# Optimization experiments

Measured on AMD Instinct MI355X. Metric: run time of the kernel, lower is better.

## Reference

```python
import jax, jax.numpy as jnp
import numpy as np

EMBED_DIM = 512
NUM_HEADS = 8
HEAD_DIM = EMBED_DIM // NUM_HEADS
GRID_SHAPE = (48, 48)
WINDOW = (16, 16)
BATCH = 2
SEQ = GRID_SHAPE[0] * GRID_SHAPE[1]
NEG = float(np.finfo(np.float16).min)  # matches torch.finfo(torch.float16).min fill


def build_window_mask():
    # replicates: indices = np.indices(grid).flatten(1).T; dist = |i-j|*2; all(dist < window)
    idx = np.indices(GRID_SHAPE).reshape(len(GRID_SHAPE), -1).T  # [N, 2]
    dist = np.abs(idx[:, None, :] - idx[None, :, :]) * 2          # [N, N, 2]
    mask = np.all(dist < np.array(WINDOW)[None, None, :], axis=-1)  # [N, N] bool
    return jnp.asarray(mask)


def setup_inputs() -> dict:
    key = jax.random.key(0)
    ks = jax.random.split(key, 11)
    s = 1.0 / np.sqrt(EMBED_DIM)
    inp = {
        "x_q": jax.random.normal(ks[0], (BATCH, SEQ, EMBED_DIM), jnp.float32),
        "x_k": jax.random.normal(ks[1], (BATCH, SEQ, EMBED_DIM), jnp.float32),
        "x_v": jax.random.normal(ks[2], (BATCH, SEQ, EMBED_DIM), jnp.float32),
        "Wq": jax.random.normal(ks[3], (EMBED_DIM, EMBED_DIM), jnp.float32) * s,
        "bq": jnp.zeros((EMBED_DIM,), jnp.float32),
        "Wk": jax.random.normal(ks[4], (EMBED_DIM, EMBED_DIM), jnp.float32) * s,
        "bk": jnp.zeros((EMBED_DIM,), jnp.float32),
        "Wv": jax.random.normal(ks[5], (EMBED_DIM, EMBED_DIM), jnp.float32) * s,
        "bv": jnp.zeros((EMBED_DIM,), jnp.float32),
        "Wo": jax.random.normal(ks[6], (EMBED_DIM, EMBED_DIM), jnp.float32) * s,
        "bo": jnp.zeros((EMBED_DIM,), jnp.float32),
        "attn_mask": build_window_mask(),
    }
    return inp


def reference(x_q, x_k, x_v, Wq, bq, Wk, bk, Wv, bv, Wo, bo, attn_mask):
    B, S, E = x_q.shape
    H, D = NUM_HEADS, HEAD_DIM

    def proj(x, W, b):
        y = x @ W.T + b                         # [B,S,E]
        return y.reshape(B, S, H, D).transpose(0, 2, 1, 3)  # [B,H,S,D]

    q = proj(x_q, Wq, bq)
    k = proj(x_k, Wk, bk)
    v = proj(x_v, Wv, bv)

    scores = jnp.einsum("bhqd,bhkd->bhqk", q, k) / np.sqrt(D)
    # Windowed branch: per-row gather over allowed keys + softmax == dense
    # softmax with disallowed keys masked to a huge negative value.
    scores = jnp.where(attn_mask[None, None, :, :], scores, NEG)
    probs = jax.nn.softmax(scores, axis=-1)     # dropout=0.0 -> identity
    context = jnp.einsum("bhqk,bhkd->bhqd", probs, v)
    context = context.transpose(0, 2, 1, 3).reshape(B, S, E)
    out = context @ Wo.T + bo
    return out
```

## Files before the change

### kernel.cpp

```cpp
#include <hip/hip_runtime.h>

typedef __attribute__((ext_vector_type(8))) short short8;
typedef __attribute__((ext_vector_type(4))) float f32x4;
typedef __attribute__((ext_vector_type(2))) unsigned int u32x2;
typedef __attribute__((ext_vector_type(4))) unsigned int u32x4;

#define DEV __device__ __forceinline__

#define QH_E 0L
#define KH_E 2359296L
#define VT_E 4718592L
#define CTX_E 7077888L

#define LOG2E 1.4426950408889634f

#define BARRIER() __builtin_amdgcn_s_barrier()
#define SCHED0() __builtin_amdgcn_sched_barrier(0)

DEV unsigned short f2bf(float f) {
  unsigned int x = __float_as_uint(f);
  x = (x + 0x7fffu + ((x >> 16) & 1u)) >> 16;
  return (unsigned short)x;
}

DEV unsigned int pk2(float a, float b) {
  unsigned int r;
  asm("v_cvt_pk_bf16_f32 %0, %1, %2" : "=v"(r) : "v"(a), "v"(b));
  return r;
}

DEV void gl2lds16(const unsigned short* g, unsigned short* l) {
  __builtin_amdgcn_global_load_lds(
      (const __attribute__((address_space(1))) unsigned int*)g,
      (__attribute__((address_space(3))) unsigned int*)l, 16, 0, 0);
}

DEV f32x4 mfma16(short8 a, short8 b, f32x4 c) {
  return __builtin_amdgcn_mfma_f32_16x16x32_bf16(a, b, c, 0, 0, 0);
}

DEV void gemm_qkv(const float* __restrict__ A, const float* __restrict__ W,
                  int m0, int n0, unsigned short* ldsA, unsigned short* ldsB,
                  f32x4 acc[2][4]) {
  const int tid = threadIdx.x;
  const int lane = tid & 63, wvv = tid >> 6;
  const int g = lane >> 4, qi = lane & 15;
  const int wr = wvv >> 1, wc = wvv & 1;
  const int c8 = tid & 7, rbase = tid >> 3;
  const int j8 = (c8 ^ (rbase & 7)) * 8;
  f32x4 ra[2][2][2];
  f32x4 rw[4][2];
#pragma unroll
  for (int mi = 0; mi < 2; ++mi)
#pragma unroll
    for (int ni = 0; ni < 4; ++ni) {
      f32x4 z = {0.f, 0.f, 0.f, 0.f};
      acc[mi][ni] = z;
    }
#define QLA(kt) do {                                                          \
    const int k0_ = (kt) * 64;                                                \
    _Pragma("unroll")                                                         \
    for (int it = 0; it < 2; ++it) {                                          \
      const float* p = A + (long)(m0 + it * 32 + rbase) * 512 + k0_ + j8;     \
      ra[(kt) & 1][it][0] = *(const f32x4*)p;                                 \
      ra[(kt) & 1][it][1] = *(const f32x4*)(p + 4);                           \
    }                                                                         \
  } while (0)
#define QLB(kt) do {                                                          \
    const int k0_ = (kt) * 64;                                                \
    _Pragma("unroll")                                                         \
    for (int it = 0; it < 4; ++it) {                                          \
      const float* p = W + (long)(n0 + it * 32 + rbase) * 512 + k0_ + j8;     \
      rw[it][0] = *(const f32x4*)p;                                           \
      rw[it][1] = *(const f32x4*)(p + 4);                                     \
    }                                                                         \
  } while (0)
#define QWA(bi, set) do {                                                     \
    _Pragma("unroll")                                                         \
    for (int it = 0; it < 2; ++it) {                                          \
      u32x4 v_;                                                               \
      v_.x = pk2(ra[set][it][0].x, ra[set][it][0].y);                         \
      v_.y = pk2(ra[set][it][0].z, ra[set][it][0].w);                         \
      v_.z = pk2(ra[set][it][1].x, ra[set][it][1].y);                         \
      v_.w = pk2(ra[set][it][1].z, ra[set][it][1].w);                         \
      *(u32x4*)(ldsA + (bi) * 4096 + (it * 256 + tid) * 8) = v_;              \
    }                                                                         \
  } while (0)
#define QWB(bi) do {                                                          \
    _Pragma("unroll")                                                         \
    for (int it = 0; it < 4; ++it) {                                          \
      u32x4 v_;                                                               \
      v_.x = pk2(rw[it][0].x, rw[it][0].y);                                   \
      v_.y = pk2(rw[it][0].z, rw[it][0].w);                                   \
      v_.z = pk2(rw[it][1].x, rw[it][1].y);                                   \
      v_.w = pk2(rw[it][1].z, rw[it][1].w);                                   \
      *(u32x4*)(ldsB + (bi) * 8192 + (it * 256 + tid) * 8) = v_;              \
    }                                                                         \
  } while (0)
  QLA(0); QLB(0);
  QWA(0, 0); QWB(0);
  QLA(1); QLB(1);
  asm volatile("s_waitcnt lgkmcnt(0)" ::: "memory");
  BARRIER();
  SCHED0();
#pragma unroll
  for (int kt = 0; kt < 8; ++kt) {
    const unsigned short* La = ldsA + (kt & 1) * 4096;
    const unsigned short* Lb = ldsB + (kt & 1) * 8192;
    __builtin_amdgcn_s_setprio(1);
#pragma unroll
    for (int kk = 0; kk < 2; ++kk) {
      short8 af[2], bfr[4];
#pragma unroll
      for (int mi = 0; mi < 2; ++mi) {
        int row = 32 * wr + 16 * mi + qi;
        int c16 = (4 * kk + g) ^ (qi & 7);
        af[mi] = *(const short8*)(La + row * 64 + c16 * 8);
      }
#pragma unroll
      for (int ni = 0; ni < 4; ++ni) {
        int row = 64 * wc + 16 * ni + qi;
        int c16 = (4 * kk + g) ^ (qi & 7);
        bfr[ni] = *(const short8*)(Lb + row * 64 + c16 * 8);
      }
#pragma unroll
      for (int mi = 0; mi < 2; ++mi)
#pragma unroll
        for (int ni = 0; ni < 4; ++ni)
          acc[mi][ni] = mfma16(af[mi], bfr[ni], acc[mi][ni]);
    }
    __builtin_amdgcn_s_setprio(0);
    SCHED0();
    if (kt < 7) { QWA((kt + 1) & 1, (kt + 1) & 1); QWB((kt + 1) & 1); }
    if (kt < 6) QLA(kt + 2);
    if (kt < 7) QLB(kt + 2);
    if (kt < 7) {
      asm volatile("s_waitcnt lgkmcnt(0)" ::: "memory");
      BARRIER();
      SCHED0();
    }
  }
#undef QLA
#undef QLB
#undef QWA
#undef QWB
}

DEV void gemm_o(const unsigned short* __restrict__ A, const float* __restrict__ W,
                int m0, int n0, unsigned short* ldsA, unsigned short* ldsB,
                f32x4 acc[2][2]) {
  const int tid = threadIdx.x;
  const int lane = tid & 63, wvv = tid >> 6;
  const int g = lane >> 4, qi = lane & 15;
  const int wr = wvv >> 1, wc = wvv & 1;
  const int c8 = tid & 7, rbase = tid >> 3;
  const int j8 = (c8 ^ (rbase & 7)) * 8;
  u32x4 rab[2][2];
  f32x4 rw[2][2][2];
#pragma unroll
  for (int mi = 0; mi < 2; ++mi)
#pragma unroll
    for (int ni = 0; ni < 2; ++ni) {
      f32x4 z = {0.f, 0.f, 0.f, 0.f};
      acc[mi][ni] = z;
    }
#define OLA(kt) do {                                                          \
    const int k0_ = (kt) * 64;                                                \
    _Pragma("unroll")                                                         \
    for (int it = 0; it < 2; ++it)                                            \
      rab[(kt) & 1][it] =                                                     \
          *(const u32x4*)(A + (long)(m0 + it * 32 + rbase) * 512 + k0_ + j8); \
  } while (0)
#define OLB(kt) do {                                                          \
    const int k0_ = (kt) * 64;                                                \
    _Pragma("unroll")                                                         \
    for (int it = 0; it < 2; ++it) {                                          \
      const float* p = W + (long)(n0 + it * 32 + rbase) * 512 + k0_ + j8;     \
      rw[(kt) & 1][it][0] = *(const f32x4*)p;                                 \
      rw[(kt) & 1][it][1] = *(const f32x4*)(p + 4);                           \
    }                                                                         \
  } while (0)
#define OW(kt) do {                                                           \
    const int b3_ = (kt) % 3, s_ = (kt) & 1;                                  \
    _Pragma("unroll")                                                         \
    for (int it = 0; it < 2; ++it)                                            \
      *(u32x4*)(ldsA + b3_ * 4096 + (it * 256 + tid) * 8) = rab[s_][it];      \
    _Pragma("unroll")                                                         \
    for (int it = 0; it < 2; ++it) {                                          \
      u32x4 v_;                                                               \
      v_.x = pk2(rw[s_][it][0].x, rw[s_][it][0].y);                           \
      v_.y = pk2(rw[s_][it][0].z, rw[s_][it][0].w);                           \
      v_.z = pk2(rw[s_][it][1].x, rw[s_][it][1].y);                           \
      v_.w = pk2(rw[s_][it][1].z, rw[s_][it][1].w);                           \
      *(u32x4*)(ldsB + b3_ * 4096 + (it * 256 + tid) * 8) = v_;               \
    }                                                                         \
  } while (0)
  OLA(0); OLB(0);
  OLA(1); OLB(1);
  OW(0);
  OLA(2); OLB(2);
  OW(1);
  OLA(3); OLB(3);
  asm volatile("s_waitcnt lgkmcnt(0)" ::: "memory");
  BARRIER();
  SCHED0();
#pragma unroll
  for (int kt = 0; kt < 8; ++kt) {
    const unsigned short* La = ldsA + (kt % 3) * 4096;
    const unsigned short* Lb = ldsB + (kt % 3) * 4096;
    __builtin_amdgcn_s_setprio(1);
#pragma unroll
    for (int kk = 0; kk < 2; ++kk) {
      short8 af[2], bfr[2];
#pragma unroll
      for (int mi = 0; mi < 2; ++mi) {
        int row = 32 * wr + 16 * mi + qi;
        int c16 = (4 * kk + g) ^ (qi & 7);
        af[mi] = *(const short8*)(La + row * 64 + c16 * 8);
      }
#pragma unroll
      for (int ni = 0; ni < 2; ++ni) {
        int row = 32 * wc + 16 * ni + qi;
        int c16 = (4 * kk + g) ^ (qi & 7);
        bfr[ni] = *(const short8*)(Lb + row * 64 + c16 * 8);
      }
#pragma unroll
      for (int mi = 0; mi < 2; ++mi)
#pragma unroll
        for (int ni = 0; ni < 2; ++ni)
          acc[mi][ni] = mfma16(af[mi], bfr[ni], acc[mi][ni]);
    }
    __builtin_amdgcn_s_setprio(0);
    SCHED0();
    if (kt < 6) OW(kt + 2);
    if (kt < 4) { OLA(kt + 4); OLB(kt + 4); }
    if (kt < 7) {
      asm volatile("s_waitcnt lgkmcnt(0)" ::: "memory");
      BARRIER();
      SCHED0();
    }
  }
#undef OLA
#undef OLB
#undef OW
}

__global__ __launch_bounds__(256, 3) void proj_qkv_kernel(
    const float* __restrict__ xq, const float* __restrict__ xk,
    const float* __restrict__ xv, const float* __restrict__ wqp,
    const float* __restrict__ wkp, const float* __restrict__ wvp,
    const float* __restrict__ bq, const float* __restrict__ bk,
    const float* __restrict__ bv, unsigned short* __restrict__ ws) {
  __shared__ unsigned short ldsA[2 * 4096];
  __shared__ unsigned short ldsB[2 * 8192];
  int f = blockIdx.x;
  int wid = (f & 7) * 108 + (f >> 3);
  const int z = wid / 288;
  const int rem = wid % 288;
  const int m0 = (rem >> 2) * 64, n0 = (rem & 3) * 128;
  const float *A, *W, *bias;
  unsigned short* dst;
  float oscale;
  int mode;
  if (z == 0)      { A = xq; W = wqp; bias = bq; oscale = 0.125f * LOG2E; dst = ws + QH_E; mode = 0; }
  else if (z == 1) { A = xk; W = wkp; bias = bk; oscale = 1.0f;           dst = ws + KH_E; mode = 0; }
  else             { A = xv; W = wvp; bias = bv; oscale = 1.0f;           dst = ws + VT_E; mode = 1; }
  f32x4 acc[2][4];
  gemm_qkv(A, W, m0, n0, ldsA, ldsB, acc);
  const int lane = threadIdx.x & 63, wvv = threadIdx.x >> 6;
  const int g = lane >> 4, qi = lane & 15;
  const int wr = wvv >> 1, wc = wvv & 1;
#pragma unroll
  for (int ni = 0; ni < 4; ++ni) {
    int n = n0 + 64 * wc + 16 * ni + qi;
    float bb = bias[n];
    int h = n >> 6, d = n & 63;
#pragma unroll
    for (int mi = 0; mi < 2; ++mi) {
      int m = m0 + 32 * wr + 16 * mi + 4 * g;
      int b = (m >= 2304) ? 1 : 0;
      int s = m - b * 2304;
      if (mode == 0) {
#pragma unroll
        for (int r = 0; r < 4; ++r) {
          float v = (acc[mi][ni][r] + bb) * oscale;
          dst[((long)((b * 8 + h) * 2304 + s + r)) * 64 + d] = f2bf(v);
        }
      } else {
        u32x2 o;
        o.x = pk2(acc[mi][ni][0] + bb, acc[mi][ni][1] + bb);
        o.y = pk2(acc[mi][ni][2] + bb, acc[mi][ni][3] + bb);
        *(u32x2*)(dst + ((long)((b * 8 + h) * 64 + d)) * 2304 + s) = o;
      }
    }
  }
}

__global__ __launch_bounds__(256, 3) void proj_out_kernel(
    const unsigned short* __restrict__ ws, const float* __restrict__ wop,
    const float* __restrict__ bo, float* __restrict__ out) {
  __shared__ unsigned short ldsA[3 * 4096];
  __shared__ unsigned short ldsB[3 * 4096];
  int f = blockIdx.x;
  int wid = (f & 7) * 72 + (f >> 3);
  const int m0 = (wid >> 3) * 64, n0 = (wid & 7) * 64;
  f32x4 acc[2][2];
  gemm_o(ws + CTX_E, wop, m0, n0, ldsA, ldsB, acc);
  const int lane = threadIdx.x & 63, wvv = threadIdx.x >> 6;
  const int g = lane >> 4, qi = lane & 15;
  const int wr = wvv >> 1, wc = wvv & 1;
#pragma unroll
  for (int ni = 0; ni < 2; ++ni) {
    int n = n0 + 32 * wc + 16 * ni + qi;
    float bb = bo[n];
#pragma unroll
    for (int mi = 0; mi < 2; ++mi) {
#pragma unroll
      for (int r = 0; r < 4; ++r) {
        int m = m0 + 32 * wr + 16 * mi + 4 * g + r;
        out[(long)m * 512 + n] = acc[mi][ni][r] + bb;
      }
    }
  }
}

__global__ __launch_bounds__(192) void attn_kernel(unsigned short* __restrict__ ws) {
  __shared__ unsigned short ldsKV[3 * 7168];
  __shared__ unsigned short ldsP[3][16][72];
  __shared__ unsigned short ldsDum[512];
  const int tid = threadIdx.x;
  const int lane = tid & 63, wv = tid >> 6;
  const int g = lane >> 4, qi = lane & 15;
  int f = blockIdx.x;
  int wid = (f & 7) * 96 + (f >> 3);
  const int bh = wid / 48, r = wid - 48 * bh;
  const int ci = wv * 16 + qi;
  const unsigned short* Kh = ws + KH_E + (long)bh * 2304 * 64;
  const unsigned short* Vt = ws + VT_E + (long)bh * 64 * 2304;
  const int q = r * 48 + ci;
  const unsigned short* qp = ws + QH_E + ((long)bh * 2304 + q) * 64;
  f32x4 qraw0 = *(const f32x4*)(qp + 8 * g);
  f32x4 qraw1 = *(const f32x4*)(qp + 32 + 8 * g);
  asm volatile("" : "+v"(qraw0), "+v"(qraw1));
  short8 qf0 = __builtin_bit_cast(short8, qraw0);
  short8 qf1 = __builtin_bit_cast(short8, qraw1);
  float msk[12];
#pragma unroll
  for (int mb = 0; mb < 3; ++mb)
#pragma unroll
    for (int rr = 0; rr < 4; ++rr) {
      int cj = 16 * mb + 4 * g + rr;
      msk[mb * 4 + rr] = ((unsigned)(ci - cj + 7) <= 14u) ? 0.f : -1e30f;
    }
  {
    u32x2 z2; z2.x = 0u; z2.y = 0u;
    *(u32x2*)(&ldsP[wv][qi][48 + 4 * g]) = z2;
  }
  f32x4 cacc[4];
#pragma unroll
  for (int mb = 0; mb < 4; ++mb) { f32x4 z = {0.f, 0.f, 0.f, 0.f}; cacc[mb] = z; }
  float lrun = 0.f;

#define ASTAGE(bi, rj) do {                                                   \
    unsigned short* Lb_ = ldsKV + (bi) * 7168;                                \
    const unsigned short* Ks_ = Kh + (long)(rj) * 3072;                       \
    _Pragma("unroll")                                                         \
    for (int it = 0; it < 5; ++it) {                                          \
      int u = it * 192 + tid;                                                 \
      if (u < 384) {                                                          \
        int kr = u >> 3, c = u & 7, cs = c ^ (kr & 7);                        \
        gl2lds16(Ks_ + kr * 64 + cs * 8, Lb_ + u * 8);                        \
      } else if (u < 896) {                                                   \
        int v2 = u - 384;                                                     \
        int d = v2 >> 3, c = v2 & 7, cs = c ^ (d & 7);                        \
        long jb = (long)(rj) * 48 + cs * 8;                                   \
        if (jb > 2296) jb = 2296;                                             \
        gl2lds16(Vt + (long)d * 2304 + jb, Lb_ + u * 8);                      \
      } else {                                                                \
        gl2lds16(Kh + (u - 896) * 8, ldsDum + (u - 896) * 8);                 \
      }                                                                       \
    }                                                                         \
  } while (0)

#define AQK(KB, S) do {                                                       \
    const unsigned short* Kt_ = (KB);                                         \
    _Pragma("unroll")                                                         \
    for (int mb = 0; mb < 3; ++mb) { f32x4 z = {0.f,0.f,0.f,0.f}; S[mb] = z; }\
    __builtin_amdgcn_s_setprio(1);                                            \
    _Pragma("unroll")                                                         \
    for (int kk = 0; kk < 2; ++kk) {                                          \
      short8 qf_ = kk ? qf1 : qf0;                                            \
      _Pragma("unroll")                                                       \
      for (int mb = 0; mb < 3; ++mb) {                                        \
        int row = 16 * mb + qi;                                               \
        int c16 = (4 * kk + g) ^ (qi & 7);                                    \
        short8 ka = *(const short8*)(Kt_ + row * 64 + c16 * 8);               \
        S[mb] = mfma16(ka, qf_, S[mb]);                                       \
      }                                                                       \
    }                                                                         \
    __builtin_amdgcn_s_setprio(0);                                            \
  } while (0)

#define ASMPV(VB, S) do {                                                     \
    const unsigned short* Vm_ = (VB);                                         \
    unsigned int pw[6];                                                       \
    _Pragma("unroll")                                                         \
    for (int mb = 0; mb < 3; ++mb) {                                          \
      float p0 = __builtin_amdgcn_exp2f(S[mb][0] + msk[mb * 4 + 0]);          \
      float p1 = __builtin_amdgcn_exp2f(S[mb][1] + msk[mb * 4 + 1]);          \
      float p2 = __builtin_amdgcn_exp2f(S[mb][2] + msk[mb * 4 + 2]);          \
      float p3 = __builtin_amdgcn_exp2f(S[mb][3] + msk[mb * 4 + 3]);          \
      lrun += (p0 + p1) + (p2 + p3);                                          \
      pw[2 * mb] = pk2(p0, p1);                                               \
      pw[2 * mb + 1] = pk2(p2, p3);                                           \
    }                                                                         \
    _Pragma("unroll")                                                         \
    for (int mb = 0; mb < 3; ++mb) {                                          \
      u32x2 pv2; pv2.x = pw[2 * mb]; pv2.y = pw[2 * mb + 1];                  \
      *(u32x2*)(&ldsP[wv][qi][16 * mb + 4 * g]) = pv2;                        \
    }                                                                         \
    __builtin_amdgcn_s_setprio(1);                                            \
    _Pragma("unroll")                                                         \
    for (int kk = 0; kk < 2; ++kk) {                                          \
      short8 pb = *(const short8*)(&ldsP[wv][qi][32 * kk + 8 * g]);           \
      _Pragma("unroll")                                                       \
      for (int mb = 0; mb < 4; ++mb) {                                        \
        int row = 16 * mb + qi;                                               \
        int c16 = (4 * kk + g) ^ (qi & 7);                                    \
        short8 va = *(const short8*)(Vm_ + row * 64 + c16 * 8);               \
        cacc[mb] = mfma16(va, pb, cacc[mb]);                                  \
      }                                                                       \
    }                                                                         \
    __builtin_amdgcn_s_setprio(0);                                            \
  } while (0)

  const int rlo = (r > 7) ? r - 7 : 0;
  const int rhi = (r < 40) ? r + 7 : 47;
  const int nch = rhi - rlo + 1;
  f32x4 sE[3], sO[3];
  ASTAGE(0, rlo);
  ASTAGE(1, rlo + 1);
  asm volatile("s_waitcnt vmcnt(5)" ::: "memory");
  BARRIER();
  SCHED0();
  AQK(ldsKV, sE);
  int bc = 0;
  for (int t = 0; t < nch; t += 2) {
    const int b1 = (bc + 1 == 3) ? 0 : bc + 1;
    const int b2 = (b1 + 1 == 3) ? 0 : b1 + 1;
    asm volatile("s_waitcnt vmcnt(0)" ::: "memory");
    BARRIER();
    SCHED0();
    if (t + 2 < nch) ASTAGE(b2, rlo + t + 2);
    if (t + 1 < nch) AQK(ldsKV + b1 * 7168, sO);
    ASMPV(ldsKV + bc * 7168 + 3072, sE);
    if (t + 1 < nch) {
      asm volatile("s_waitcnt vmcnt(0)" ::: "memory");
      BARRIER();
      SCHED0();
      if (t + 3 < nch) ASTAGE(bc, rlo + t + 3);
      if (t + 2 < nch) AQK(ldsKV + b2 * 7168, sE);
      ASMPV(ldsKV + b1 * 7168 + 3072, sO);
    }
    bc = b2;
  }
#undef ASTAGE
#undef AQK
#undef ASMPV
  lrun += __shfl_xor(lrun, 16);
  lrun += __shfl_xor(lrun, 32);
  const float inv = 1.0f / lrun;
  unsigned short* ctx = ws + CTX_E;
  const int b2w = bh >> 3, h2 = bh & 7;
#pragma unroll
  for (int mb = 0; mb < 4; ++mb) {
    u32x2 o;
    o.x = pk2(cacc[mb][0] * inv, cacc[mb][1] * inv);
    o.y = pk2(cacc[mb][2] * inv, cacc[mb][3] * inv);
    long off = ((long)(b2w * 2304 + q)) * 512 + h2 * 64 + 16 * mb + 4 * g;
    *(u32x2*)(ctx + off) = o;
  }
}

extern "C" void kernel_launch(void* const* d_in, const int* in_sizes, int n_in,
                              void* d_out, int out_size, void* d_ws, size_t ws_size,
                              hipStream_t stream) {
  const float* xq = (const float*)d_in[0];
  const float* xk = (const float*)d_in[1];
  const float* xv = (const float*)d_in[2];
  const float* wq = (const float*)d_in[3];
  const float* bq = (const float*)d_in[4];
  const float* wk = (const float*)d_in[5];
  const float* bk = (const float*)d_in[6];
  const float* wv = (const float*)d_in[7];
  const float* bv = (const float*)d_in[8];
  const float* wo = (const float*)d_in[9];
  const float* bo = (const float*)d_in[10];
  unsigned short* ws = (unsigned short*)d_ws;
  float* out = (float*)d_out;

  proj_qkv_kernel<<<dim3(864), dim3(256), 0, stream>>>(xq, xk, xv, wq, wk, wv,
                                                       bq, bk, bv, ws);
  attn_kernel<<<dim3(768), dim3(192), 0, stream>>>(ws);
  proj_out_kernel<<<dim3(576), dim3(256), 0, stream>>>(ws, wo, bo, out);
}
```

Baseline: 58.76 us.

## Rewrite QKV projection as LDS-free single-wave kernel loading MFMA fragments directly

The QKV projection GEMM no longer stages tiles through double-buffered shared memory with barriers. Each 64-thread block now computes a 32x64 tile, loading fp32 operands from global memory straight into MFMA fragment layout, converting to bf16 in registers, and software-pipelining the loads over two register sets. This removes LDS traffic and block-wide synchronisation. In exchange, data reuse across waves is lost, so operands are re-read from global or L2 more often, and the per-lane loads are less coalesced.

Measured after the change: 122.6 us. +108.7%, slower.

```diff
diff --git a/kernel.cpp b/kernel.cpp
--- a/kernel.cpp
+++ b/kernel.cpp
@@ -39,111 +39,111 @@
   return __builtin_amdgcn_mfma_f32_16x16x32_bf16(a, b, c, 0, 0, 0);
 }
 
-DEV void gemm_qkv(const float* __restrict__ A, const float* __restrict__ W,
-                  int m0, int n0, unsigned short* ldsA, unsigned short* ldsB,
-                  f32x4 acc[2][4]) {
-  const int tid = threadIdx.x;
-  const int lane = tid & 63, wvv = tid >> 6;
+__global__ __launch_bounds__(64) void proj_qkv_kernel(
+    const float* __restrict__ xq, const float* __restrict__ xk,
+    const float* __restrict__ xv, const float* __restrict__ wqp,
+    const float* __restrict__ wkp, const float* __restrict__ wvp,
+    const float* __restrict__ bq, const float* __restrict__ bk,
+    const float* __restrict__ bv, unsigned short* __restrict__ ws) {
+  int f = blockIdx.x;
+  int wid = (f & 7) * 432 + (f >> 3);
+  const int z = wid / 1152;
+  const int rem = wid % 1152;
+  const int m0 = (rem >> 3) * 32, n0 = (rem & 7) * 64;
+  const float *A, *W, *bias;
+  unsigned short* dst;
+  float oscale;
+  int mode;
+  if (z == 0)      { A = xq; W = wqp; bias = bq; oscale = 0.125f * LOG2E; dst = ws + QH_E; mode = 0; }
+  else if (z == 1) { A = xk; W = wkp; bias = bk; oscale = 1.0f;           dst = ws + KH_E; mode = 0; }
+  else             { A = xv; W = wvp; bias = bv; oscale = 1.0f;           dst = ws + VT_E; mode = 1; }
+  const int lane = threadIdx.x;
   const int g = lane >> 4, qi = lane & 15;
-  const int wr = wvv >> 1, wc = wvv & 1;
-  const int c8 = tid & 7, rbase = tid >> 3;
-  const int j8 = (c8 ^ (rbase & 7)) * 8;
-  f32x4 ra[2][2][2];
-  f32x4 rw[4][2];
+  const float* Ab = A + (long)(m0 + qi) * 512 + 8 * g;
+  const float* Wb = W + (long)(n0 + qi) * 512 + 8 * g;
+  f32x4 acc[2][4];
 #pragma unroll
   for (int mi = 0; mi < 2; ++mi)
 #pragma unroll
     for (int ni = 0; ni < 4; ++ni) {
-      f32x4 z = {0.f, 0.f, 0.f, 0.f};
-      acc[mi][ni] = z;
-    }
-#define QLA(kt) do {                                                          \
-    const int k0_ = (kt) * 64;                                                \
-    _Pragma("unroll")                                                         \
-    for (int it = 0; it < 2; ++it) {                                          \
-      const float* p = A + (long)(m0 + it * 32 + rbase) * 512 + k0_ + j8;     \
-      ra[(kt) & 1][it][0] = *(const f32x4*)p;                                 \
-      ra[(kt) & 1][it][1] = *(const f32x4*)(p + 4);                           \
-    }                                                                         \
-  } while (0)
-#define QLB(kt) do {                                                          \
-    const int k0_ = (kt) * 64;                                                \
-    _Pragma("unroll")                                                         \
-    for (int it = 0; it < 4; ++it) {                                          \
-      const float* p = W + (long)(n0 + it * 32 + rbase) * 512 + k0_ + j8;     \
-      rw[it][0] = *(const f32x4*)p;                                           \
-      rw[it][1] = *(const f32x4*)(p + 4);                                     \
-    }                                                                         \
-  } while (0)
-#define QWA(bi, set) do {                                                     \
-    _Pragma("unroll")                                                         \
-    for (int it = 0; it < 2; ++it) {                                          \
+      f32x4 z4 = {0.f, 0.f, 0.f, 0.f};
+      acc[mi][ni] = z4;
+    }
+  f32x4 ea[2][2], ew[4][2], oa[2][2], ow[4][2];
+#define QLD(AR, WR, s) do {                                                   \
+    _Pragma("unroll")                                                         \
+    for (int mi = 0; mi < 2; ++mi) {                                          \
+      const float* p_ = Ab + mi * (16 * 512) + (s) * 32;                      \
+      AR[mi][0] = *(const f32x4*)p_;                                          \
+      AR[mi][1] = *(const f32x4*)(p_ + 4);                                    \
+    }                                                                         \
+    _Pragma("unroll")                                                         \
+    for (int ni = 0; ni < 4; ++ni) {                                          \
+      const float* p_ = Wb + ni * (16 * 512) + (s) * 32;                      \
+      WR[ni][0] = *(const f32x4*)p_;                                          \
+      WR[ni][1] = *(const f32x4*)(p_ + 4);                                    \
+    }                                                                         \
+  } while (0)
+#define QCM(AR, WR) do {                                                      \
+    short8 af_[2], bw_[4];                                                    \
+    _Pragma("unroll")                                                         \
+    for (int mi = 0; mi < 2; ++mi) {                                          \
       u32x4 v_;                                                               \
-      v_.x = pk2(ra[set][it][0].x, ra[set][it][0].y);                         \
-      v_.y = pk2(ra[set][it][0].z, ra[set][it][0].w);                         \
-      v_.z = pk2(ra[set][it][1].x, ra[set][it][1].y);                         \
-      v_.w = pk2(ra[set][it][1].z, ra[set][it][1].w);                         \
-      *(u32x4*)(ldsA + (bi) * 4096 + (it * 256 + tid) * 8) = v_;              \
-    }                                                                         \
-  } while (0)
-#define QWB(bi) do {                                                          \
-    _Pragma("unroll")                                                         \
-    for (int it = 0; it < 4; ++it) {                                          \
+      v_.x = pk2(AR[mi][0].x, AR[mi][0].y);                                   \
+      v_.y = pk2(AR[mi][0].z, AR[mi][0].w);                                   \
+      v_.z = pk2(AR[mi][1].x, AR[mi][1].y);                                   \
+      v_.w = pk2(AR[mi][1].z, AR[mi][1].w);                                   \
+      af_[mi] = __builtin_bit_cast(short8, v_);                               \
+    }                                                                         \
+    _Pragma("unroll")                                                         \
+    for (int ni = 0; ni < 4; ++ni) {                                          \
       u32x4 v_;                                                               \
-      v_.x = pk2(rw[it][0].x, rw[it][0].y);                                   \
-      v_.y = pk2(rw[it][0].z, rw[it][0].w);                                   \
-      v_.z = pk2(rw[it][1].x, rw[it][1].y);                                   \
-      v_.w = pk2(rw[it][1].z, rw[it][1].w);                                   \
-      *(u32x4*)(ldsB + (bi) * 8192 + (it * 256 + tid) * 8) = v_;              \
-    }                                                                         \
-  } while (0)
-  QLA(0); QLB(0);
-  QWA(0, 0); QWB(0);
-  QLA(1); QLB(1);
-  asm volatile("s_waitcnt lgkmcnt(0)" ::: "memory");
-  BARRIER();
-  SCHED0();
-#pragma unroll
-  for (int kt = 0; kt < 8; ++kt) {
-    const unsigned short* La = ldsA + (kt & 1) * 4096;
-    const unsigned short* Lb = ldsB + (kt & 1) * 8192;
-    __builtin_amdgcn_s_setprio(1);
-#pragma unroll
-    for (int kk = 0; kk < 2; ++kk) {
-      short8 af[2], bfr[4];
-#pragma unroll
-      for (int mi = 0; mi < 2; ++mi) {
-        int row = 32 * wr + 16 * mi + qi;
-        int c16 = (4 * kk + g) ^ (qi & 7);
-        af[mi] = *(const short8*)(La + row * 64 + c16 * 8);
+      v_.x = pk2(WR[ni][0].x, WR[ni][0].y);                                   \
+      v_.y = pk2(WR[ni][0].z, WR[ni][0].w);                                   \
+      v_.z = pk2(WR[ni][1].x, WR[ni][1].y);                                   \
+      v_.w = pk2(WR[ni][1].z, WR[ni][1].w);                                   \
+      bw_[ni] = __builtin_bit_cast(short8, v_);                               \
+    }                                                                         \
+    _Pragma("unroll")                                                         \
+    for (int mi = 0; mi < 2; ++mi)                                            \
+      _Pragma("unroll")                                                       \
+      for (int ni = 0; ni < 4; ++ni)                                          \
+        acc[mi][ni] = mfma16(af_[mi], bw_[ni], acc[mi][ni]);                  \
+  } while (0)
+  QLD(ea, ew, 0);
+#pragma unroll
+  for (int s = 0; s < 16; s += 2) {
+    QLD(oa, ow, s + 1);
+    QCM(ea, ew);
+    if (s + 2 < 16) QLD(ea, ew, s + 2);
+    QCM(oa, ow);
+  }
+#undef QLD
+#undef QCM
+#pragma unroll
+  for (int ni = 0; ni < 4; ++ni) {
+    int n = n0 + 16 * ni + qi;
+    float bb = bias[n];
+    int h = n >> 6, d = n & 63;
+#pragma unroll
+    for (int mi = 0; mi < 2; ++mi) {
+      int m = m0 + 16 * mi + 4 * g;
+      int b = (m >= 2304) ? 1 : 0;
+      int s = m - b * 2304;
+      if (mode == 0) {
+#pragma unroll
+        for (int r = 0; r < 4; ++r) {
+          float v = (acc[mi][ni][r] + bb) * oscale;
+          dst[((long)((b * 8 + h) * 2304 + s + r)) * 64 + d] = f2bf(v);
+        }
+      } else {
+        u32x2 o;
+        o.x = pk2(acc[mi][ni][0] + bb, acc[mi][ni][1] + bb);
+        o.y = pk2(acc[mi][ni][2] + bb, acc[mi][ni][3] + bb);
+        *(u32x2*)(dst + ((long)((b * 8 + h) * 64 + d)) * 2304 + s) = o;
       }
-#pragma unroll
-      for (int ni = 0; ni < 4; ++ni) {
-        int row = 64 * wc + 16 * ni + qi;
-        int c16 = (4 * kk + g) ^ (qi & 7);
-        bfr[ni] = *(const short8*)(Lb + row * 64 + c16 * 8);
-      }
-#pragma unroll
-      for (int mi = 0; mi < 2; ++mi)
-#pragma unroll
-        for (int ni = 0; ni < 4; ++ni)
-          acc[mi][ni] = mfma16(af[mi], bfr[ni], acc[mi][ni]);
-    }
-    __builtin_amdgcn_s_setprio(0);
-    SCHED0();
-    if (kt < 7) { QWA((kt + 1) & 1, (kt + 1) & 1); QWB((kt + 1) & 1); }
-    if (kt < 6) QLA(kt + 2);
-    if (kt < 7) QLB(kt + 2);
-    if (kt < 7) {
-      asm volatile("s_waitcnt lgkmcnt(0)" ::: "memory");
-      BARRIER();
-      SCHED0();
-    }
-  }
-#undef QLA
-#undef QLB
-#undef QWA
-#undef QWB
+    }
+  }
 }
 
 DEV void gemm_o(const unsigned short* __restrict__ A, const float* __restrict__ W,
@@ -243,57 +243,6 @@
 #undef OLA
 #undef OLB
 #undef OW
-}
-
-__global__ __launch_bounds__(256, 3) void proj_qkv_kernel(
-    const float* __restrict__ xq, const float* __restrict__ xk,
-    const float* __restrict__ xv, const float* __restrict__ wqp,
-    const float* __restrict__ wkp, const float* __restrict__ wvp,
-    const float* __restrict__ bq, const float* __restrict__ bk,
-    const float* __restrict__ bv, unsigned short* __restrict__ ws) {
-  __shared__ unsigned short ldsA[2 * 4096];
-  __shared__ unsigned short ldsB[2 * 8192];
-  int f = blockIdx.x;
-  int wid = (f & 7) * 108 + (f >> 3);
-  const int z = wid / 288;
-  const int rem = wid % 288;
-  const int m0 = (rem >> 2) * 64, n0 = (rem & 3) * 128;
-  const float *A, *W, *bias;
-  unsigned short* dst;
-  float oscale;
-  int mode;
-  if (z == 0)      { A = xq; W = wqp; bias = bq; oscale = 0.125f * LOG2E; dst = ws + QH_E; mode = 0; }
-  else if (z == 1) { A = xk; W = wkp; bias = bk; oscale = 1.0f;           dst = ws + KH_E; mode = 0; }
-  else             { A = xv; W = wvp; bias = bv; oscale = 1.0f;           dst = ws + VT_E; mode = 1; }
-  f32x4 acc[2][4];
-  gemm_qkv(A, W, m0, n0, ldsA, ldsB, acc);
-  const int lane = threadIdx.x & 63, wvv = threadIdx.x >> 6;
-  const int g = lane >> 4, qi = lane & 15;
-  const int wr = wvv >> 1, wc = wvv & 1;
-#pragma unroll
-  for (int ni = 0; ni < 4; ++ni) {
-    int n = n0 + 64 * wc + 16 * ni + qi;
-    float bb = bias[n];
-    int h = n >> 6, d = n & 63;
-#pragma unroll
-    for (int mi = 0; mi < 2; ++mi) {
-      int m = m0 + 32 * wr + 16 * mi + 4 * g;
-      int b = (m >= 2304) ? 1 : 0;
-      int s = m - b * 2304;
-      if (mode == 0) {
-#pragma unroll
-        for (int r = 0; r < 4; ++r) {
-          float v = (acc[mi][ni][r] + bb) * oscale;
-          dst[((long)((b * 8 + h) * 2304 + s + r)) * 64 + d] = f2bf(v);
-        }
-      } else {
-        u32x2 o;
-        o.x = pk2(acc[mi][ni][0] + bb, acc[mi][ni][1] + bb);
-        o.y = pk2(acc[mi][ni][2] + bb, acc[mi][ni][3] + bb);
-        *(u32x2*)(dst + ((long)((b * 8 + h) * 64 + d)) * 2304 + s) = o;
-      }
-    }
-  }
 }
 
 __global__ __launch_bounds__(256, 3) void proj_out_kernel(
@@ -499,7 +448,7 @@
   unsigned short* ws = (unsigned short*)d_ws;
   float* out = (float*)d_out;
 
-  proj_qkv_kernel<<<dim3(864), dim3(256), 0, stream>>>(xq, xk, xv, wq, wk, wv,
+  proj_qkv_kernel<<<dim3(3456), dim3(64), 0, stream>>>(xq, xk, xv, wq, wk, wv,
                                                        bq, bk, bv, ws);
   attn_kernel<<<dim3(768), dim3(192), 0, stream>>>(ws);
   proj_out_kernel<<<dim3(576), dim3(256), 0, stream>>>(ws, wo, bo, out);
```
